# Performance work log

Hardware: AMD Instinct MI355X
Metric: run time of the kernel (lower is better)

The kernel has to match this reference:

```python
import jax, jax.numpy as jnp
import numpy as np

HIDDEN_STATE_CLAMP = 4.0
MAX_REVIEW_LENGTH = 200
B, T, D_IN, D_H, D_OUT = 1024, 200, 300, 256, 2


def setup_inputs() -> dict:
    key = jax.random.key(0)
    k_x, k_wh, k_bh, k_wo, k_bo = jax.random.split(key, 5)
    fan_h = D_IN + D_H
    inputs = jax.random.normal(k_x, (B, T, D_IN), dtype=jnp.float32)
    # torch nn.Linear init: U(-1/sqrt(fan_in), 1/sqrt(fan_in)); stored as [in, out] here
    Wh = jax.random.uniform(k_wh, (fan_h, D_H), jnp.float32, -1.0, 1.0) / np.sqrt(fan_h)
    bh = jax.random.uniform(k_bh, (D_H,), jnp.float32, -1.0, 1.0) / np.sqrt(fan_h)
    Wo = jax.random.uniform(k_wo, (D_H, D_OUT), jnp.float32, -1.0, 1.0) / np.sqrt(D_H)
    bo = jax.random.uniform(k_bo, (D_OUT,), jnp.float32, -1.0, 1.0) / np.sqrt(D_H)
    return {"inputs": inputs, "Wh": Wh, "bh": bh, "Wo": Wo, "bo": bo}


def reference(inputs, Wh, bh, Wo, bo):
    # inputs: [B, T, D_in]; process at most MAX_REVIEW_LENGTH timesteps
    x_t = jnp.swapaxes(inputs[:, :MAX_REVIEW_LENGTH], 0, 1)  # [T, B, D_in]
    h0 = jnp.zeros((inputs.shape[0], Wh.shape[1]), dtype=inputs.dtype)

    def step(h, xt):
        combined = jnp.concatenate([xt, h], axis=-1)          # [B, D_in+D_h]
        pre = combined @ Wh + bh
        h = jnp.tanh(jnp.clip(pre, -HIDDEN_STATE_CLAMP, HIDDEN_STATE_CLAMP))
        return h, None

    h_final, _ = jax.lax.scan(step, h0, x_t)
    pre_out = jnp.clip(h_final @ Wo + bo, -HIDDEN_STATE_CLAMP, HIDDEN_STATE_CLAMP)
    return jax.nn.log_softmax(pre_out, axis=-1)
```

## Files before the change

### kernel.cpp

```cpp
#include <hip/hip_runtime.h>
#include <stdint.h>


typedef short s16x8 __attribute__((ext_vector_type(8)));
typedef float f32x4 __attribute__((ext_vector_type(4)));

__device__ __forceinline__ unsigned short f2bf(float f){
  uint32_t u = __builtin_bit_cast(uint32_t, f);
  u += 0x7fffu + ((u >> 16) & 1u);
  return (unsigned short)(u >> 16);
}
__device__ __forceinline__ float bf2f(unsigned short s){
  uint32_t u = ((uint32_t)s) << 16;
  return __builtin_bit_cast(float, u);
}
__device__ __forceinline__ uint32_t pack2(float a, float b){
  return (uint32_t)f2bf(a) | ((uint32_t)f2bf(b) << 16);
}

__global__ void prep_kernel(const float* __restrict__ Wh,
                            unsigned short* __restrict__ wxf,
                            unsigned short* __restrict__ whhf){
  int id = blockIdx.x * 256 + threadIdx.x;
  if (id < 81920){
    int j = id & 7, lane = (id >> 3) & 63, rem = id >> 9;
    int ki = rem % 10, CT = rem / 10;
    int k = ki * 32 + ((lane >> 4) << 3) + j;
    int col = CT * 16 + (lane & 15);
    wxf[id] = (k < 300) ? f2bf(Wh[k * 256 + col]) : (unsigned short)0;
  } else if (id < 81920 + 65536){
    int id2 = id - 81920;
    int j = id2 & 7, lane = (id2 >> 3) & 63, rem = id2 >> 9;
    int ki = rem & 7, CT = rem >> 3;
    int k = ki * 32 + ((lane >> 4) << 3) + j;
    int col = CT * 16 + (lane & 15);
    whhf[id2] = f2bf(Wh[(300 + k) * 256 + col]);
  }
}

__global__ __launch_bounds__(512, 4) void phase1_kernel(
    const float* __restrict__ x, const float* __restrict__ bh,
    const unsigned short* __restrict__ wxf, unsigned short* __restrict__ U){
  __shared__ unsigned short hx[128 * 320];
  int blk = blockIdx.x;
  int bt = blk / 25;
  int t0 = (blk - bt * 25) * 8;
  int tid = threadIdx.x;
  int w = tid >> 6, l = tid & 63;
  int m = l & 15, kg = l >> 4;

  const float4* xb = (const float4*)x + (long)(bt * 16) * 15000 + t0 * 75;
  for (int i = tid; i < 9600; i += 512){
    int bl = i / 600;
    int j  = i - bl * 600;
    float4 v = xb[(long)bl * 15000 + j];
    int tt = j / 75;
    int k4 = j - tt * 75;
    int idx = (((tt * 16 + bl) * 320) + k4 * 4) ^ ((bl & 7) << 3);
    *(uint2*)(&hx[idx]) = make_uint2(pack2(v.x, v.y), pack2(v.z, v.w));
  }
  for (int i = tid; i < 640; i += 512){
    int r = i / 5, q = i - r * 5;
    int idx = (r * 320 + 300 + q * 4) ^ ((r & 7) << 3);
    *(uint2*)(&hx[idx]) = make_uint2(0u, 0u);
  }

  s16x8 Bf0[10], Bf1[10];
  const unsigned short* w0p = wxf + (2 * w + 0) * 5120 + l * 8;
  const unsigned short* w1p = wxf + (2 * w + 1) * 5120 + l * 8;
#pragma unroll
  for (int ki = 0; ki < 10; ki++){
    Bf0[ki] = *(const s16x8*)(w0p + ki * 512);
    Bf1[ki] = *(const s16x8*)(w1p + ki * 512);
  }
  float4 bv0 = *(const float4*)(bh + (2 * w + 0) * 16 + kg * 4);
  float4 bv1 = *(const float4*)(bh + (2 * w + 1) * 16 + kg * 4);
  __syncthreads();

  int abase = m * 320 + kg * 8;
  int swz = (m & 7) << 3;
#pragma unroll 1
  for (int tt = 0; tt < 8; tt++){
    f32x4 acc0 = {bv0.x, bv0.y, bv0.z, bv0.w};
    f32x4 acc1 = {bv1.x, bv1.y, bv1.z, bv1.w};
    int ab = tt * 5120 + abase;
#pragma unroll
    for (int ki = 0; ki < 10; ki++){
      s16x8 a = *(const s16x8*)(&hx[(ab + ki * 32) ^ swz]);
      acc0 = __builtin_amdgcn_mfma_f32_16x16x32_bf16(Bf0[ki], a, acc0, 0, 0, 0);
      acc1 = __builtin_amdgcn_mfma_f32_16x16x32_bf16(Bf1[ki], a, acc1, 0, 0, 0);
    }
    long base = (long)(bt * 200 + t0 + tt) * 4096;
    uint4 s;
    s.x = pack2(acc0[0], acc0[1]);
    s.y = pack2(acc0[2], acc0[3]);
    s.z = pack2(acc1[0], acc1[1]);
    s.w = pack2(acc1[2], acc1[3]);
    *(uint4*)(U + base + w * 512 + l * 8) = s;
  }
}

__global__ __launch_bounds__(512, 2) void phase2_kernel(
    const unsigned short* __restrict__ U, const unsigned short* __restrict__ whhf,
    const float* __restrict__ Wo, const float* __restrict__ bo,
    float* __restrict__ out){
  __shared__ unsigned short h2[2][16 * 272];
  __shared__ float flds[16][272];
  int bt = blockIdx.x;
  int tid = threadIdx.x;
  int w = tid >> 6, l = tid & 63;
  int n = l & 15, kg = l >> 4;

  s16x8 Bf0[8], Bf1[8];
#pragma unroll
  for (int ki = 0; ki < 8; ki++){
    Bf0[ki] = *(const s16x8*)(whhf + ((2 * w + 0) * 8 + ki) * 512 + l * 8);
    Bf1[ki] = *(const s16x8*)(whhf + ((2 * w + 1) * 8 + ki) * 512 + l * 8);
  }

  for (int i = tid; i < 16 * 272; i += 512) h2[0][i] = 0;

  const unsigned short* ub = U + (long)bt * 819200 + w * 512 + l * 8;
  s16x8 u[4];
  u[0] = *(const s16x8*)(ub);
  u[1] = *(const s16x8*)(ub + 4096);
  __syncthreads();

  float hv[8];
  int p = 0;
  for (int tq = 0; tq < 50; ++tq){
#pragma unroll
    for (int ki = 0; ki < 8; ki++){
      asm volatile("" : "+v"(Bf0[ki]), "+v"(Bf1[ki]));
    }
#pragma unroll
    for (int s = 0; s < 4; ++s){
      int t = tq * 4 + s;
      int tf = (t < 198) ? t + 2 : 199;
      u[(s + 2) & 3] = *(const s16x8*)(ub + (long)tf * 4096);

      s16x8 a[8];
#pragma unroll
      for (int ki = 0; ki < 8; ki++)
        a[ki] = *(const s16x8*)(&h2[p][n * 272 + ki * 32 + kg * 8]);

      f32x4 acc0a, acc1a;
      f32x4 acc0b = {0.f, 0.f, 0.f, 0.f}, acc1b = {0.f, 0.f, 0.f, 0.f};
#pragma unroll
      for (int r = 0; r < 4; r++){
        acc0a[r] = bf2f((unsigned short)u[s][r]);
        acc1a[r] = bf2f((unsigned short)u[s][4 + r]);
      }
#pragma unroll
      for (int ki = 0; ki < 4; ki++){
        acc0a = __builtin_amdgcn_mfma_f32_16x16x32_bf16(Bf0[ki],     a[ki],     acc0a, 0, 0, 0);
        acc1a = __builtin_amdgcn_mfma_f32_16x16x32_bf16(Bf1[ki],     a[ki],     acc1a, 0, 0, 0);
        acc0b = __builtin_amdgcn_mfma_f32_16x16x32_bf16(Bf0[ki + 4], a[ki + 4], acc0b, 0, 0, 0);
        acc1b = __builtin_amdgcn_mfma_f32_16x16x32_bf16(Bf1[ki + 4], a[ki + 4], acc1b, 0, 0, 0);
      }
#pragma unroll
      for (int i = 0; i < 8; i++){
        float pre = (i < 4) ? (acc0a[i] + acc0b[i]) : (acc1a[i - 4] + acc1b[i - 4]);
        float c = fminf(fmaxf(pre, -4.f), 4.f);
        float e = __expf(2.f * c);
        hv[i] = 1.f - 2.f * __builtin_amdgcn_rcpf(e + 1.f);
      }
      {
        uint2 d0 = make_uint2(pack2(hv[0], hv[1]), pack2(hv[2], hv[3]));
        uint2 d1 = make_uint2(pack2(hv[4], hv[5]), pack2(hv[6], hv[7]));
        *(uint2*)(&h2[p ^ 1][n * 272 + (2 * w + 0) * 16 + kg * 4]) = d0;
        *(uint2*)(&h2[p ^ 1][n * 272 + (2 * w + 1) * 16 + kg * 4]) = d1;
      }
      __syncthreads();
      p ^= 1;
    }
  }

#pragma unroll
  for (int i = 0; i < 8; i++){
    int r = i & 3, c = i >> 2;
    flds[n][(2 * w + c) * 16 + kg * 4 + r] = hv[i];
  }
  __syncthreads();
  int row = tid >> 5, q = tid & 31;
  float p0 = 0.f, p1 = 0.f;
#pragma unroll
  for (int jj = 0; jj < 8; jj++){
    float hvv = flds[row][q + 32 * jj];
    p0 += hvv * Wo[(q + 32 * jj) * 2 + 0];
    p1 += hvv * Wo[(q + 32 * jj) * 2 + 1];
  }
#pragma unroll
  for (int mm = 16; mm >= 1; mm >>= 1){
    p0 += __shfl_xor(p0, mm, 32);
    p1 += __shfl_xor(p1, mm, 32);
  }
  if (q == 0){
    p0 = fminf(fmaxf(p0 + bo[0], -4.f), 4.f);
    p1 = fminf(fmaxf(p1 + bo[1], -4.f), 4.f);
    float mx = fmaxf(p0, p1);
    float lse = mx + logf(__expf(p0 - mx) + __expf(p1 - mx));
    int orow = bt * 16 + row;
    out[orow * 2 + 0] = p0 - lse;
    out[orow * 2 + 1] = p1 - lse;
  }
}

extern "C" void kernel_launch(void* const* d_in, const int* in_sizes, int n_in,
                              void* d_out, int out_size, void* d_ws, size_t ws_size,
                              hipStream_t stream){
  const float* x  = (const float*)d_in[0];
  const float* Wh = (const float*)d_in[1];
  const float* bh = (const float*)d_in[2];
  const float* Wo = (const float*)d_in[3];
  const float* bo = (const float*)d_in[4];
  float* out = (float*)d_out;

  unsigned short* U    = (unsigned short*)d_ws;
  unsigned short* wxf  = (unsigned short*)((char*)d_ws + 104857600);
  unsigned short* whhf = (unsigned short*)((char*)d_ws + 104857600 + 163840);

  prep_kernel<<<576, 256, 0, stream>>>(Wh, wxf, whhf);
  phase1_kernel<<<1600, 512, 0, stream>>>(x, bh, wxf, U);
  phase2_kernel<<<64, 512, 0, stream>>>(U, whhf, Wo, bo, out);
}
```

Before: 236.6 us.

## Fold tanh exp scaling into weights, drop clamp, swizzle LDS, single accumulator chain

Pre-scales the weights and bias by 2*log2(e) so the recurrent step can use exp2 directly. The clamp is removed, on the reasoning that tanh saturates anyway. The two split accumulator chains are merged into one serial chain of eight MFMAs per output tile, and the LDS hidden-state buffers get an XOR swizzle to avoid bank conflicts. bf16 packing switches to a cheaper round-half-up perm, and the buffer index is made compile-time via s&1. The goal is fewer VALU ops on the serial recurrence, at the cost of a longer MFMA dependency chain and slightly different rounding.

```diff
diff --git a/kernel.cpp b/kernel.cpp
--- a/kernel.cpp
+++ b/kernel.cpp
@@ -4,6 +4,8 @@
 
 typedef short s16x8 __attribute__((ext_vector_type(8)));
 typedef float f32x4 __attribute__((ext_vector_type(4)));
+
+#define SCL  2.8853900817779268f
 
 __device__ __forceinline__ unsigned short f2bf(float f){
   uint32_t u = __builtin_bit_cast(uint32_t, f);
@@ -16,6 +18,11 @@
 }
 __device__ __forceinline__ uint32_t pack2(float a, float b){
   return (uint32_t)f2bf(a) | ((uint32_t)f2bf(b) << 16);
+}
+__device__ __forceinline__ uint32_t pkrhu(float lo, float hi){
+  uint32_t a = __builtin_bit_cast(uint32_t, lo) + 0x8000u;
+  uint32_t b = __builtin_bit_cast(uint32_t, hi) + 0x8000u;
+  return __builtin_amdgcn_perm(b, a, 0x07060302u);
 }
 
 __global__ void prep_kernel(const float* __restrict__ Wh,
@@ -27,14 +34,14 @@
     int ki = rem % 10, CT = rem / 10;
     int k = ki * 32 + ((lane >> 4) << 3) + j;
     int col = CT * 16 + (lane & 15);
-    wxf[id] = (k < 300) ? f2bf(Wh[k * 256 + col]) : (unsigned short)0;
+    wxf[id] = (k < 300) ? f2bf(SCL * Wh[k * 256 + col]) : (unsigned short)0;
   } else if (id < 81920 + 65536){
     int id2 = id - 81920;
     int j = id2 & 7, lane = (id2 >> 3) & 63, rem = id2 >> 9;
     int ki = rem & 7, CT = rem >> 3;
     int k = ki * 32 + ((lane >> 4) << 3) + j;
     int col = CT * 16 + (lane & 15);
-    whhf[id2] = f2bf(Wh[(300 + k) * 256 + col]);
+    whhf[id2] = f2bf(SCL * Wh[(300 + k) * 256 + col]);
   }
 }
 
@@ -75,6 +82,8 @@
   }
   float4 bv0 = *(const float4*)(bh + (2 * w + 0) * 16 + kg * 4);
   float4 bv1 = *(const float4*)(bh + (2 * w + 1) * 16 + kg * 4);
+  bv0.x *= SCL; bv0.y *= SCL; bv0.z *= SCL; bv0.w *= SCL;
+  bv1.x *= SCL; bv1.y *= SCL; bv1.z *= SCL; bv1.w *= SCL;
   __syncthreads();
 
   int abase = m * 320 + kg * 8;
@@ -110,6 +119,7 @@
   int tid = threadIdx.x;
   int w = tid >> 6, l = tid & 63;
   int n = l & 15, kg = l >> 4;
+  int sw = ((n >> 2) & 1) << 3;
 
   s16x8 Bf0[8], Bf1[8];
 #pragma unroll
@@ -126,8 +136,10 @@
   u[1] = *(const s16x8*)(ub + 4096);
   __syncthreads();
 
+  int rbase = (n * 272 + kg * 8) ^ sw;
+  int wbase = (n * 272 + kg * 4) ^ sw;
+
   float hv[8];
-  int p = 0;
   for (int tq = 0; tq < 50; ++tq){
 #pragma unroll
     for (int ki = 0; ki < 8; ki++){
@@ -142,37 +154,32 @@
       s16x8 a[8];
 #pragma unroll
       for (int ki = 0; ki < 8; ki++)
-        a[ki] = *(const s16x8*)(&h2[p][n * 272 + ki * 32 + kg * 8]);
-
-      f32x4 acc0a, acc1a;
-      f32x4 acc0b = {0.f, 0.f, 0.f, 0.f}, acc1b = {0.f, 0.f, 0.f, 0.f};
+        a[ki] = *(const s16x8*)(&h2[s & 1][rbase + ki * 32]);
+
+      f32x4 acc0, acc1;
 #pragma unroll
       for (int r = 0; r < 4; r++){
-        acc0a[r] = bf2f((unsigned short)u[s][r]);
-        acc1a[r] = bf2f((unsigned short)u[s][4 + r]);
-      }
-#pragma unroll
-      for (int ki = 0; ki < 4; ki++){
-        acc0a = __builtin_amdgcn_mfma_f32_16x16x32_bf16(Bf0[ki],     a[ki],     acc0a, 0, 0, 0);
-        acc1a = __builtin_amdgcn_mfma_f32_16x16x32_bf16(Bf1[ki],     a[ki],     acc1a, 0, 0, 0);
-        acc0b = __builtin_amdgcn_mfma_f32_16x16x32_bf16(Bf0[ki + 4], a[ki + 4], acc0b, 0, 0, 0);
-        acc1b = __builtin_amdgcn_mfma_f32_16x16x32_bf16(Bf1[ki + 4], a[ki + 4], acc1b, 0, 0, 0);
+        acc0[r] = bf2f((unsigned short)u[s][r]);
+        acc1[r] = bf2f((unsigned short)u[s][4 + r]);
+      }
+#pragma unroll
+      for (int ki = 0; ki < 8; ki++){
+        acc0 = __builtin_amdgcn_mfma_f32_16x16x32_bf16(Bf0[ki], a[ki], acc0, 0, 0, 0);
+        acc1 = __builtin_amdgcn_mfma_f32_16x16x32_bf16(Bf1[ki], a[ki], acc1, 0, 0, 0);
       }
 #pragma unroll
       for (int i = 0; i < 8; i++){
-        float pre = (i < 4) ? (acc0a[i] + acc0b[i]) : (acc1a[i - 4] + acc1b[i - 4]);
-        float c = fminf(fmaxf(pre, -4.f), 4.f);
-        float e = __expf(2.f * c);
-        hv[i] = 1.f - 2.f * __builtin_amdgcn_rcpf(e + 1.f);
+        float v = (i < 4) ? acc0[i] : acc1[i - 4];
+        float e = __builtin_amdgcn_exp2f(v);
+        hv[i] = fmaf(-2.f, __builtin_amdgcn_rcpf(e + 1.f), 1.f);
       }
       {
-        uint2 d0 = make_uint2(pack2(hv[0], hv[1]), pack2(hv[2], hv[3]));
-        uint2 d1 = make_uint2(pack2(hv[4], hv[5]), pack2(hv[6], hv[7]));
-        *(uint2*)(&h2[p ^ 1][n * 272 + (2 * w + 0) * 16 + kg * 4]) = d0;
-        *(uint2*)(&h2[p ^ 1][n * 272 + (2 * w + 1) * 16 + kg * 4]) = d1;
+        uint2 d0 = make_uint2(pkrhu(hv[0], hv[1]), pkrhu(hv[2], hv[3]));
+        uint2 d1 = make_uint2(pkrhu(hv[4], hv[5]), pkrhu(hv[6], hv[7]));
+        *(uint2*)(&h2[(s & 1) ^ 1][wbase + (2 * w + 0) * 16]) = d0;
+        *(uint2*)(&h2[(s & 1) ^ 1][wbase + (2 * w + 1) * 16]) = d1;
       }
       __syncthreads();
-      p ^= 1;
     }
   }
 
```

Result: faster. 206.4 us (-12.7%).
